# Performance work log

Measured on AMD Instinct MI355X. Metric: run time of the kernel, lower is better.

## Reference

```python
import jax, jax.numpy as jnp
import numpy as np

HIDDEN = 768
HEADS = 12
HEAD_DIM = HIDDEN // HEADS
NORM = float(np.sqrt(HIDDEN))  # module divides by sqrt(hidden_size), not sqrt(head_dim)


def setup_inputs() -> dict:
    key = jax.random.key(0)
    ks = jax.random.split(key, 7)
    B, S, H = 8, 1024, HIDDEN
    scale = 0.02
    return {
        "hidden_states": jax.random.normal(ks[0], (B, S, H), dtype=jnp.float32),
        "Wq": jax.random.normal(ks[1], (H, H), dtype=jnp.float32) * scale,
        "bq": jax.random.normal(ks[2], (H,), dtype=jnp.float32) * scale,
        "Wk": jax.random.normal(ks[3], (H, H), dtype=jnp.float32) * scale,
        "bk": jax.random.normal(ks[4], (H,), dtype=jnp.float32) * scale,
        "Wv": jax.random.normal(ks[5], (H, H), dtype=jnp.float32) * scale,
        "bv": jax.random.normal(ks[6], (H,), dtype=jnp.float32) * scale,
    }


def reference(hidden_states, Wq, bq, Wk, bk, Wv, bv):
    B, S, H = hidden_states.shape
    def heads(x):  # [B,S,H] -> [B,nh,S,hd]
        return x.reshape(B, S, HEADS, HEAD_DIM).transpose(0, 2, 1, 3)
    q = heads(hidden_states @ Wq + bq)
    k = heads(hidden_states @ Wk + bk)
    v = heads(hidden_states @ Wv + bv)
    # naive quadratic attention (world_size=1 ring): scores materialized
    scores = jnp.einsum("bhqd,bhkd->bhqk", q, k) / NORM
    probs = jax.nn.softmax(scores, axis=-1)  # dropout prob = 0.0
    ctx = jnp.einsum("bhqk,bhkd->bhqd", probs, v)
    # [B,nh,S,hd] -> [B,S,H]
    return ctx.transpose(0, 2, 1, 3).reshape(B, S, H)
```

## Files before the change

### kernel.cpp

```cpp
#include <hip/hip_runtime.h>
#include <hip/hip_bf16.h>
#include <stdint.h>

typedef __attribute__((ext_vector_type(8))) short short8;
typedef __attribute__((ext_vector_type(4))) float f32x4;
typedef __attribute__((ext_vector_type(4))) int i32x4;
typedef __attribute__((ext_vector_type(2))) int i32x2;
typedef __attribute__((ext_vector_type(4))) unsigned short u16x4;

#define HIDDEN 768
#define HEADS 12
#define HD 64
#define NB 8
#define SEQ 1024
#define MTOT (NB*SEQ)
#define QSCALE 0.05205887314427834f

typedef const __attribute__((address_space(1))) uint32_t* gas1_t;
typedef __attribute__((address_space(3))) uint32_t* las3_t;
#define GL_LDS16(g, l) __builtin_amdgcn_global_load_lds((gas1_t)(g), (las3_t)(l), 16, 0, 0)

static __device__ __forceinline__ unsigned short f2bf(float f){
  uint32_t u = __builtin_bit_cast(uint32_t, f);
  u += 0x7fffu + ((u >> 16) & 1u);
  return (unsigned short)(u >> 16);
}
static __device__ __forceinline__ float fexp2(float x){
#if __has_builtin(__builtin_amdgcn_exp2f)
  return __builtin_amdgcn_exp2f(x);
#else
  return exp2f(x);
#endif
}

__global__ void convert_x_kernel(const float* __restrict__ x, unsigned short* __restrict__ xb){
  int i = blockIdx.x * 256 + threadIdx.x;
  float4 v = reinterpret_cast<const float4*>(x)[i];
  u16x4 o;
  o[0]=f2bf(v.x); o[1]=f2bf(v.y); o[2]=f2bf(v.z); o[3]=f2bf(v.w);
  reinterpret_cast<u16x4*>(xb)[i] = o;
}

__global__ void transpose_w_kernel(const float* __restrict__ Wq, const float* __restrict__ Wk,
                                   const float* __restrict__ Wv, unsigned short* __restrict__ Wt){
  __shared__ float t[32][33];
  int z = blockIdx.z;
  const float* W = (z==0) ? Wq : ((z==1) ? Wk : Wv);
  unsigned short* o = Wt + (size_t)z * HIDDEN * HIDDEN;
  int n0 = blockIdx.x * 32, k0 = blockIdx.y * 32;
  int x = threadIdx.x & 31, y0 = threadIdx.x >> 5;
#pragma unroll
  for(int p=0;p<4;p++){ int y = y0 + p*8; t[y][x] = W[(size_t)(k0+y)*HIDDEN + n0 + x]; }
  __syncthreads();
#pragma unroll
  for(int p=0;p<4;p++){ int y = y0 + p*8; o[(size_t)(n0+y)*HIDDEN + k0 + x] = f2bf(t[x][y]); }
}

__global__ __launch_bounds__(256, 4) void gemm_qkv_kernel(
    const unsigned short* __restrict__ Xb, const unsigned short* __restrict__ Wt,
    const float* __restrict__ bq, const float* __restrict__ bk, const float* __restrict__ bv,
    unsigned short* __restrict__ Qg, unsigned short* __restrict__ Kg, unsigned short* __restrict__ Vt)
{
  __shared__ alignas(16) unsigned short lA[128*64];
  __shared__ alignas(16) unsigned short lB[128*64];
  int wgid = blockIdx.x;
  int xcd = wgid & 7, idx = wgid >> 3;
  int y = xcd + 8*(idx/18);
  int within = idx % 18;
  int xb = within % 6, z = within / 6;
  const unsigned short* W = Wt + (size_t)z*HIDDEN*HIDDEN;
  const float* bias = (z==0) ? bq : ((z==1) ? bk : bv);
  int m0 = y * 128, n0 = xb * 128;
  int tid = threadIdx.x;
  int w = tid >> 6, lane = tid & 63, l16 = lane & 15, g = lane >> 4;
  int wm = w >> 1, wn = w & 1;
  f32x4 acc[4][4] = {};
  for(int kt=0; kt<HIDDEN; kt+=64){
    __syncthreads();
#pragma unroll
    for(int p=0;p<4;p++){
      int t2 = p*256 + tid;
      int r = t2 >> 3;
      int cb = (((t2 & 7) << 4) ^ ((r & 7) << 4));
      GL_LDS16(Xb + (size_t)(m0 + r)*HIDDEN + kt + (cb >> 1), lA + p*2048 + w*512);
      GL_LDS16(W  + (size_t)(n0 + r)*HIDDEN + kt + (cb >> 1), lB + p*2048 + w*512);
    }
    __syncthreads();
#pragma unroll
    for(int kk=0;kk<2;kk++){
      short8 af[4], bf[4];
#pragma unroll
      for(int i=0;i<4;i++){
        int row = wm*64 + i*16 + l16;
        af[i] = *reinterpret_cast<const short8*>(
            reinterpret_cast<const unsigned char*>(lA) + row*128 + ((kk*64 + g*16) ^ ((row&7)<<4)));
      }
#pragma unroll
      for(int j=0;j<4;j++){
        int row = wn*64 + j*16 + l16;
        bf[j] = *reinterpret_cast<const short8*>(
            reinterpret_cast<const unsigned char*>(lB) + row*128 + ((kk*64 + g*16) ^ ((row&7)<<4)));
      }
#pragma unroll
      for(int i=0;i<4;i++)
#pragma unroll
        for(int j=0;j<4;j++)
          acc[i][j] = __builtin_amdgcn_mfma_f32_16x16x32_bf16(af[i], bf[j], acc[i][j], 0, 0, 0);
    }
  }
  if(z == 2){
#pragma unroll
    for(int i=0;i<4;i++){
      int mb = m0 + wm*64 + i*16 + g*4;
      int b = mb >> 10, s = mb & 1023;
#pragma unroll
      for(int j=0;j<4;j++){
        int n = n0 + wn*64 + j*16 + l16;
        float bi = bias[n];
        int h = n >> 6, d = n & 63;
        u16x4 pk;
#pragma unroll
        for(int r=0;r<4;r++) pk[r] = f2bf(acc[i][j][r] + bi);
        *reinterpret_cast<u16x4*>(Vt + ((size_t)(b*HEADS + h)*HD + d)*SEQ + s) = pk;
      }
    }
  } else {
    unsigned short* out = (z==0) ? Qg : Kg;
#pragma unroll
    for(int i=0;i<4;i++){
      int mb = m0 + wm*64 + i*16 + g*4;
#pragma unroll
      for(int j=0;j<4;j++){
        int n = n0 + wn*64 + j*16 + l16;
        float bi = bias[n];
        int h = n >> 6, d = n & 63;
#pragma unroll
        for(int r=0;r<4;r++){
          int m = mb + r;
          int b = m >> 10, s = m & 1023;
          float cv = acc[i][j][r] + bi;
          if(z == 0) cv *= QSCALE;
          out[((size_t)(b*HEADS + h)*SEQ + s)*HD + d] = f2bf(cv);
        }
      }
    }
  }
}

__global__ __launch_bounds__(256, 3) void attn_kernel(
    const unsigned short* __restrict__ Qg, const unsigned short* __restrict__ Kg,
    const unsigned short* __restrict__ Vt, float* __restrict__ out)
{
  __shared__ alignas(16) unsigned short lK[2][64*64];
  __shared__ alignas(16) unsigned short lV[2][64*64];
  int wgid = blockIdx.x;
  int xcd = wgid & 7, ix = wgid >> 3;
  int bh = xcd*12 + (ix >> 3), qb = ix & 7;
  int b = bh / HEADS, h = bh % HEADS;
  int tid = threadIdx.x, w = tid >> 6, lane = tid & 63, l16 = lane & 15, g = lane >> 4;

  const unsigned short* Qbase = Qg + ((size_t)bh*SEQ + qb*128 + w*32)*HD;
  short8 qA0 = *reinterpret_cast<const short8*>(Qbase + l16*HD + g*8);
  short8 qA1 = *reinterpret_cast<const short8*>(Qbase + l16*HD + 32 + g*8);
  short8 qB0 = *reinterpret_cast<const short8*>(Qbase + (16+l16)*HD + g*8);
  short8 qB1 = *reinterpret_cast<const short8*>(Qbase + (16+l16)*HD + 32 + g*8);

  f32x4 oacc[2][4] = {};
  float lpart[2] = {0.f, 0.f};

  int sw = (l16 & 7) << 4;
  int ro0 = l16*128 + ((g*16) ^ sw);
  int ro1 = l16*128 + ((64 + g*16) ^ sw);
  int vo00 = l16*128 + ((      8*g) ^ sw);
  int vo01 = l16*128 + ((32  + 8*g) ^ sw);
  int vo10 = l16*128 + ((64  + 8*g) ^ sw);
  int vo11 = l16*128 + ((96  + 8*g) ^ sw);
  const unsigned char* lKb = reinterpret_cast<const unsigned char*>(&lK[0][0]);
  const unsigned char* lVb = reinterpret_cast<const unsigned char*>(&lV[0][0]);

  int r0 = tid >> 3;
  int cb0 = (((tid & 7) << 4) ^ ((r0 & 7) << 4)) >> 1;
  const unsigned short* gK0 = Kg + (size_t)bh*SEQ*HD + r0*HD + cb0;
  const unsigned short* gV0 = Vt + (size_t)bh*HD*SEQ + r0*SEQ + cb0;

#define STAGE(B, t) do { \
    GL_LDS16(gK0 + (t)*4096,          &lK[B][0] + w*512); \
    GL_LDS16(gK0 + (t)*4096 + 2048,   &lK[B][0] + 2048 + w*512); \
    GL_LDS16(gV0 + (t)*64,            &lV[B][0] + w*512); \
    GL_LDS16(gV0 + (t)*64 + 32*SEQ,   &lV[B][0] + 2048 + w*512); \
  } while(0)

#define SMPV(SREG, LP, OA) do { \
    int Wlo[4], Whi[4]; \
    _Pragma("unroll") for(int j=0;j<4;j++){ \
      float p0=fexp2(SREG[j][0]), p1=fexp2(SREG[j][1]); \
      float p2=fexp2(SREG[j][2]), p3=fexp2(SREG[j][3]); \
      LP += (p0+p1)+(p2+p3); \
      asm("v_cvt_pk_bf16_f32 %0, %1, %2" : "=v"(Wlo[j]) : "v"(p0), "v"(p1)); \
      asm("v_cvt_pk_bf16_f32 %0, %1, %2" : "=v"(Whi[j]) : "v"(p2), "v"(p3)); } \
    _Pragma("unroll") for(int m=0;m<2;m++){ \
      i32x4 cc; cc[0]=Wlo[2*m]; cc[1]=Whi[2*m]; cc[2]=Wlo[2*m+1]; cc[3]=Whi[2*m+1]; \
      short8 pB = __builtin_bit_cast(short8, cc); \
      _Pragma("unroll") for(int jn=0;jn<4;jn++) \
        OA[jn] = __builtin_amdgcn_mfma_f32_16x16x32_bf16(vf[jn][m], pB, OA[jn], 0,0,0); } \
  } while(0)

#define TILE(CUR, kt, HAS_NEXT) do { \
    if(HAS_NEXT) STAGE((CUR)^1, (kt)+1); \
    short8 kf[4][2]; \
    _Pragma("unroll") for(int j=0;j<4;j++){ \
      kf[j][0] = *reinterpret_cast<const short8*>(lKb + (CUR)*8192 + j*2048 + ro0); \
      kf[j][1] = *reinterpret_cast<const short8*>(lKb + (CUR)*8192 + j*2048 + ro1); } \
    short8 vf[4][2]; \
    _Pragma("unroll") for(int jn=0;jn<4;jn++){ \
      { i32x2 vl = *reinterpret_cast<const i32x2*>(lVb + (CUR)*8192 + jn*2048 + vo00); \
        i32x2 vh = *reinterpret_cast<const i32x2*>(lVb + (CUR)*8192 + jn*2048 + vo01); \
        i32x4 vc; vc[0]=vl[0]; vc[1]=vl[1]; vc[2]=vh[0]; vc[3]=vh[1]; \
        vf[jn][0] = __builtin_bit_cast(short8, vc); } \
      { i32x2 vl = *reinterpret_cast<const i32x2*>(lVb + (CUR)*8192 + jn*2048 + vo10); \
        i32x2 vh = *reinterpret_cast<const i32x2*>(lVb + (CUR)*8192 + jn*2048 + vo11); \
        i32x4 vc; vc[0]=vl[0]; vc[1]=vl[1]; vc[2]=vh[0]; vc[3]=vh[1]; \
        vf[jn][1] = __builtin_bit_cast(short8, vc); } } \
    f32x4 s0[4], s1[4]; \
    _Pragma("unroll") for(int j=0;j<4;j++){ \
      f32x4 zz = {}; \
      zz    = __builtin_amdgcn_mfma_f32_16x16x32_bf16(kf[j][0], qA0, zz, 0,0,0); \
      s0[j] = __builtin_amdgcn_mfma_f32_16x16x32_bf16(kf[j][1], qA1, zz, 0,0,0); } \
    _Pragma("unroll") for(int j=0;j<4;j++){ \
      f32x4 zz = {}; \
      zz    = __builtin_amdgcn_mfma_f32_16x16x32_bf16(kf[j][0], qB0, zz, 0,0,0); \
      s1[j] = __builtin_amdgcn_mfma_f32_16x16x32_bf16(kf[j][1], qB1, zz, 0,0,0); } \
    SMPV(s0, lpart[0], oacc[0]); \
    SMPV(s1, lpart[1], oacc[1]); \
    __syncthreads(); \
  } while(0)

  STAGE(0, 0);
  __syncthreads();

  for(int kt=0; kt<SEQ/64; kt+=2){
    TILE(0, kt, true);
    TILE(1, kt+1, (kt+1) < SEQ/64 - 1);
  }

#pragma unroll
  for(int rg=0;rg<2;rg++){
    float tot = lpart[rg];
    tot += __shfl_xor(tot, 16, 64);
    tot += __shfl_xor(tot, 32, 64);
    float invl = 1.0f / tot;
    int s = qb*128 + w*32 + rg*16 + l16;
    float* orow = out + ((size_t)b*SEQ + s)*HIDDEN + h*HD + 4*g;
#pragma unroll
    for(int jn=0;jn<4;jn++){
      float4 val;
      val.x = oacc[rg][jn][0]*invl; val.y = oacc[rg][jn][1]*invl;
      val.z = oacc[rg][jn][2]*invl; val.w = oacc[rg][jn][3]*invl;
      *reinterpret_cast<float4*>(orow + 16*jn) = val;
    }
  }
#undef STAGE
#undef SMPV
#undef TILE
}

extern "C" void kernel_launch(void* const* d_in, const int* in_sizes, int n_in,
                              void* d_out, int out_size, void* d_ws, size_t ws_size,
                              hipStream_t stream) {
  const float* hs = (const float*)d_in[0];
  const float* Wq = (const float*)d_in[1];
  const float* bq = (const float*)d_in[2];
  const float* Wk = (const float*)d_in[3];
  const float* bk = (const float*)d_in[4];
  const float* Wv = (const float*)d_in[5];
  const float* bv = (const float*)d_in[6];
  float* out = (float*)d_out;

  char* ws = (char*)d_ws;
  unsigned short* Xb = (unsigned short*)ws;
  unsigned short* Wt = (unsigned short*)(ws + (size_t)12582912);
  unsigned short* Qg = (unsigned short*)(ws + (size_t)16121856);
  unsigned short* Kg = Qg + (size_t)MTOT*HIDDEN;
  unsigned short* Vt = Kg + (size_t)MTOT*HIDDEN;

  convert_x_kernel<<<MTOT*HIDDEN/4/256, 256, 0, stream>>>(hs, Xb);
  transpose_w_kernel<<<dim3(24,24,3), 256, 0, stream>>>(Wq, Wk, Wv, Wt);
  gemm_qkv_kernel<<<1152, 256, 0, stream>>>(Xb, Wt, bq, bk, bv, Qg, Kg, Vt);
  attn_kernel<<<768, 256, 0, stream>>>(Qg, Kg, Vt, out);
}
```

Baseline: 88.23 us.

## Fuse fp32-to-bf16 input conversion into QKV GEMM with double-buffered LDS

Drops the separate convert_x kernel. The QKV GEMM now loads fp32 hidden states directly, converts them to bf16 in registers with v_cvt_pk_bf16_f32 and writes them to swizzled LDS. LDS is double-buffered so the loads for the next K-tile overlap the MFMA compute on the current one, with one barrier per iteration. This removes a full read-write pass over X and one kernel launch, but each GEMM block reads fp32 X (twice the bytes), repeats the conversion across the N tiles, and uses more LDS with occupancy dropped to 2.

```diff
diff --git a/kernel.cpp b/kernel.cpp
--- a/kernel.cpp
+++ b/kernel.cpp
@@ -31,14 +31,6 @@
 #else
   return exp2f(x);
 #endif
-}
-
-__global__ void convert_x_kernel(const float* __restrict__ x, unsigned short* __restrict__ xb){
-  int i = blockIdx.x * 256 + threadIdx.x;
-  float4 v = reinterpret_cast<const float4*>(x)[i];
-  u16x4 o;
-  o[0]=f2bf(v.x); o[1]=f2bf(v.y); o[2]=f2bf(v.z); o[3]=f2bf(v.w);
-  reinterpret_cast<u16x4*>(xb)[i] = o;
 }
 
 __global__ void transpose_w_kernel(const float* __restrict__ Wq, const float* __restrict__ Wk,
@@ -56,13 +48,13 @@
   for(int p=0;p<4;p++){ int y = y0 + p*8; o[(size_t)(n0+y)*HIDDEN + k0 + x] = f2bf(t[x][y]); }
 }
 
-__global__ __launch_bounds__(256, 4) void gemm_qkv_kernel(
-    const unsigned short* __restrict__ Xb, const unsigned short* __restrict__ Wt,
+__global__ __launch_bounds__(256, 2) void gemm_qkv_kernel(
+    const float* __restrict__ Xf, const unsigned short* __restrict__ Wt,
     const float* __restrict__ bq, const float* __restrict__ bk, const float* __restrict__ bv,
     unsigned short* __restrict__ Qg, unsigned short* __restrict__ Kg, unsigned short* __restrict__ Vt)
 {
-  __shared__ alignas(16) unsigned short lA[128*64];
-  __shared__ alignas(16) unsigned short lB[128*64];
+  __shared__ alignas(16) unsigned short lA[2][128*64];
+  __shared__ alignas(16) unsigned short lB[2][128*64];
   int wgid = blockIdx.x;
   int xcd = wgid & 7, idx = wgid >> 3;
   int y = xcd + 8*(idx/18);
@@ -74,40 +66,68 @@
   int tid = threadIdx.x;
   int w = tid >> 6, lane = tid & 63, l16 = lane & 15, g = lane >> 4;
   int wm = w >> 1, wn = w & 1;
+
+  const float* XA = Xf + (size_t)(m0 + (tid>>3))*HIDDEN + (tid&7)*8;
+  int awoff = (tid>>3)*128 + (((tid&7)*16) ^ (((tid>>3)&7)<<4));
+  int cbB = ((((tid&7)<<4) ^ (((tid>>3)&7)<<4)) >> 1);
+  const unsigned short* gB0 = W + (size_t)(n0 + (tid>>3))*HIDDEN + cbB;
+  int swr = (l16 & 7) << 4;
+  int oA = (wm*64 + l16)*128;
+  int oB = (wn*64 + l16)*128;
+  int ok0 = (g*16) ^ swr, ok1 = (64 + g*16) ^ swr;
+  const unsigned char* lAb = reinterpret_cast<const unsigned char*>(&lA[0][0]);
+  const unsigned char* lBb = reinterpret_cast<const unsigned char*>(&lB[0][0]);
+
   f32x4 acc[4][4] = {};
-  for(int kt=0; kt<HIDDEN; kt+=64){
+
+#define LOADA(A0, A1, t) do { _Pragma("unroll") for(int p=0;p<4;p++){ \
+    const float4* s = reinterpret_cast<const float4*>(XA + (size_t)p*32*HIDDEN + (t)*64); \
+    A0[p] = s[0]; A1[p] = s[1]; } } while(0)
+
+#define WRITEA(B, A0, A1) do { _Pragma("unroll") for(int p=0;p<4;p++){ \
+    i32x4 pk; \
+    asm("v_cvt_pk_bf16_f32 %0, %1, %2" : "=v"(pk[0]) : "v"(A0[p].x), "v"(A0[p].y)); \
+    asm("v_cvt_pk_bf16_f32 %0, %1, %2" : "=v"(pk[1]) : "v"(A0[p].z), "v"(A0[p].w)); \
+    asm("v_cvt_pk_bf16_f32 %0, %1, %2" : "=v"(pk[2]) : "v"(A1[p].x), "v"(A1[p].y)); \
+    asm("v_cvt_pk_bf16_f32 %0, %1, %2" : "=v"(pk[3]) : "v"(A1[p].z), "v"(A1[p].w)); \
+    *reinterpret_cast<i32x4*>(reinterpret_cast<unsigned char*>(&lA[B][0]) + awoff + p*4096) = pk; \
+  } } while(0)
+
+#define STAGEB(B, t) do { _Pragma("unroll") for(int p=0;p<4;p++) \
+    GL_LDS16(gB0 + (size_t)p*32*HIDDEN + (t)*64, &lB[B][0] + p*2048 + w*512); } while(0)
+
+#define COMPUTE(CUR) do { _Pragma("unroll") for(int kk=0;kk<2;kk++){ \
+    short8 af[4], bf[4]; \
+    int okk = kk ? ok1 : ok0; \
+    _Pragma("unroll") for(int i=0;i<4;i++) \
+      af[i] = *reinterpret_cast<const short8*>(lAb + (CUR)*16384 + oA + i*2048 + okk); \
+    _Pragma("unroll") for(int j=0;j<4;j++) \
+      bf[j] = *reinterpret_cast<const short8*>(lBb + (CUR)*16384 + oB + j*2048 + okk); \
+    _Pragma("unroll") for(int i=0;i<4;i++) \
+      _Pragma("unroll") for(int j=0;j<4;j++) \
+        acc[i][j] = __builtin_amdgcn_mfma_f32_16x16x32_bf16(af[i], bf[j], acc[i][j], 0, 0, 0); \
+  } } while(0)
+
+  {
+    float4 a0[4], a1[4];
+    LOADA(a0, a1, 0);
+    STAGEB(0, 0);
+    WRITEA(0, a0, a1);
+  }
+  __syncthreads();
+
+  for(int t=0; t<12; t++){
+    int cur = t & 1;
+    float4 a0[4], a1[4];
+    if(t < 11){
+      LOADA(a0, a1, t+1);
+      STAGEB(cur^1, t+1);
+    }
+    COMPUTE(cur);
+    if(t < 11) WRITEA(cur^1, a0, a1);
     __syncthreads();
-#pragma unroll
-    for(int p=0;p<4;p++){
-      int t2 = p*256 + tid;
-      int r = t2 >> 3;
-      int cb = (((t2 & 7) << 4) ^ ((r & 7) << 4));
-      GL_LDS16(Xb + (size_t)(m0 + r)*HIDDEN + kt + (cb >> 1), lA + p*2048 + w*512);
-      GL_LDS16(W  + (size_t)(n0 + r)*HIDDEN + kt + (cb >> 1), lB + p*2048 + w*512);
-    }
-    __syncthreads();
-#pragma unroll
-    for(int kk=0;kk<2;kk++){
-      short8 af[4], bf[4];
-#pragma unroll
-      for(int i=0;i<4;i++){
-        int row = wm*64 + i*16 + l16;
-        af[i] = *reinterpret_cast<const short8*>(
-            reinterpret_cast<const unsigned char*>(lA) + row*128 + ((kk*64 + g*16) ^ ((row&7)<<4)));
-      }
-#pragma unroll
-      for(int j=0;j<4;j++){
-        int row = wn*64 + j*16 + l16;
-        bf[j] = *reinterpret_cast<const short8*>(
-            reinterpret_cast<const unsigned char*>(lB) + row*128 + ((kk*64 + g*16) ^ ((row&7)<<4)));
-      }
-#pragma unroll
-      for(int i=0;i<4;i++)
-#pragma unroll
-        for(int j=0;j<4;j++)
-          acc[i][j] = __builtin_amdgcn_mfma_f32_16x16x32_bf16(af[i], bf[j], acc[i][j], 0, 0, 0);
-    }
-  }
+  }
+
   if(z == 2){
 #pragma unroll
     for(int i=0;i<4;i++){
@@ -145,6 +165,10 @@
       }
     }
   }
+#undef LOADA
+#undef WRITEA
+#undef STAGEB
+#undef COMPUTE
 }
 
 __global__ __launch_bounds__(256, 3) void attn_kernel(
@@ -277,14 +301,12 @@
   float* out = (float*)d_out;
 
   char* ws = (char*)d_ws;
-  unsigned short* Xb = (unsigned short*)ws;
-  unsigned short* Wt = (unsigned short*)(ws + (size_t)12582912);
-  unsigned short* Qg = (unsigned short*)(ws + (size_t)16121856);
+  unsigned short* Wt = (unsigned short*)ws;
+  unsigned short* Qg = (unsigned short*)(ws + (size_t)4*1024*1024);
   unsigned short* Kg = Qg + (size_t)MTOT*HIDDEN;
   unsigned short* Vt = Kg + (size_t)MTOT*HIDDEN;
 
-  convert_x_kernel<<<MTOT*HIDDEN/4/256, 256, 0, stream>>>(hs, Xb);
   transpose_w_kernel<<<dim3(24,24,3), 256, 0, stream>>>(Wq, Wk, Wv, Wt);
-  gemm_qkv_kernel<<<1152, 256, 0, stream>>>(Xb, Wt, bq, bk, bv, Qg, Kg, Vt);
+  gemm_qkv_kernel<<<1152, 256, 0, stream>>>(hs, Wt, bq, bk, bv, Qg, Kg, Vt);
   attn_kernel<<<768, 256, 0, stream>>>(Qg, Kg, Vt, out);
 }
```

New measurement: 102.6 us. +16.2%, slower.
